# Kernel tuning notes

Measured on AMD Instinct MI355X. Metric: run time of the kernel, lower is better.

## Reference

```python
import jax, jax.numpy as jnp
from jax import lax
import numpy as np

B, T, F, H, C = 2048, 200, 64, 128, 1
IN = 2 * F + H  # GRUCell input size


def setup_inputs() -> dict:
    key = jax.random.key(0)
    ks = jax.random.split(key, 16)
    sd_h = 1.0 / np.sqrt(H)
    sd_f = 1.0 / np.sqrt(F)
    sd_g = 1.0 / np.sqrt(H)
    return {
        "values": jax.random.normal(ks[0], (B, T, F), jnp.float32),
        "masks": jnp.round(jax.random.uniform(ks[1], (B, T, F), jnp.float32)),
        "deltas": jax.random.uniform(ks[2], (B, T, F), jnp.float32),
        "x_locf": jax.random.normal(ks[3], (B, T, F), jnp.float32),
        "emp_mean": jax.random.normal(ks[4], (F,), jnp.float32),
        "Wdh": jax.random.uniform(ks[5], (H, F), jnp.float32, -sd_h, sd_h),
        "bdh": jax.random.uniform(ks[6], (H,), jnp.float32, -sd_h, sd_h),
        "Wdx": jax.random.uniform(ks[7], (F, F), jnp.float32, -sd_f, sd_f),
        "bdx": jax.random.uniform(ks[8], (F,), jnp.float32, -sd_f, sd_f),
        "w_ih": jax.random.uniform(ks[9], (3 * H, IN), jnp.float32, -sd_g, sd_g),
        "w_hh": jax.random.uniform(ks[10], (3 * H, H), jnp.float32, -sd_g, sd_g),
        "b_ih": jax.random.uniform(ks[11], (3 * H,), jnp.float32, -sd_g, sd_g),
        "b_hh": jax.random.uniform(ks[12], (3 * H,), jnp.float32, -sd_g, sd_g),
        "Wc": jax.random.uniform(ks[13], (C, H), jnp.float32, -sd_g, sd_g),
        "bc": jax.random.uniform(ks[14], (C,), jnp.float32, -sd_g, sd_g),
    }


def reference(values, masks, deltas, x_locf, emp_mean,
              Wdh, bdh, Wdx, bdx, w_ih, w_hh, b_ih, b_hh, Wc, bc):
    # GRU-D forward: sequential scan over time with temporal decay gating.
    eye = jnp.eye(Wdx.shape[0], dtype=Wdx.dtype)
    Wdx_diag = Wdx * eye  # diag=True TemporalDecay

    def step(h, inp):
        x, m, d, xl = inp  # each [B, F]
        gamma_h = jnp.exp(-jax.nn.relu(d @ Wdh.T + bdh))   # [B, H]
        gamma_x = jnp.exp(-jax.nn.relu(d @ Wdx_diag.T + bdx))  # [B, F]
        h = h * gamma_h
        x_h = gamma_x * xl + (1.0 - gamma_x) * emp_mean
        x_rep = m * x + (1.0 - m) * x_h
        inputs = jnp.concatenate([x_rep, h, m], axis=1)    # [B, 2F+H]
        gi = inputs @ w_ih.T + b_ih                        # [B, 3H]
        gh = h @ w_hh.T + b_hh                             # [B, 3H]
        i_r, i_z, i_n = jnp.split(gi, 3, axis=1)
        h_r, h_z, h_n = jnp.split(gh, 3, axis=1)
        r = jax.nn.sigmoid(i_r + h_r)
        z = jax.nn.sigmoid(i_z + h_z)
        n = jnp.tanh(i_n + r * h_n)
        h_new = (1.0 - z) * n + z * h
        return h_new, None

    xs = (values.transpose(1, 0, 2), masks.transpose(1, 0, 2),
          deltas.transpose(1, 0, 2), x_locf.transpose(1, 0, 2))
    h0 = jnp.zeros((values.shape[0], Wdh.shape[0]), values.dtype)
    h_final, _ = lax.scan(step, h0, xs)
    logits = h_final @ Wc.T + bc
    return jax.nn.sigmoid(logits)
```

## Files before the change

### kernel.cpp

```cpp
#include <hip/hip_runtime.h>
#include <hip/hip_bf16.h>

#define Bsz 2048
#define Tn  200
#define Fn  64
#define Hn  128
#define INn 256
#define Gn  384
#define BBn 8

typedef __bf16 bf16x8 __attribute__((ext_vector_type(8)));
typedef float  f32x4  __attribute__((ext_vector_type(4)));

__device__ __forceinline__ float sigm(float x)  { return 1.f / (1.f + __expf(-x)); }
__device__ __forceinline__ float tanh_(float x) { return 1.f - 2.f / (__expf(2.f * x) + 1.f); }

__global__ __launch_bounds__(512, 2) void grud_scan(
    const float* __restrict__ values, const float* __restrict__ masks,
    const float* __restrict__ deltas, const float* __restrict__ x_locf,
    const float* __restrict__ emp_mean,
    const float* __restrict__ Wdh, const float* __restrict__ bdh,
    const float* __restrict__ Wdx, const float* __restrict__ bdx,
    const float* __restrict__ w_ih, const float* __restrict__ w_hh,
    const float* __restrict__ b_ih, const float* __restrict__ b_hh,
    const float* __restrict__ Wc, const float* __restrict__ bc,
    float* __restrict__ out)
{
    __shared__ __align__(16) __bf16 in_bf[16][INn + 8];
    __shared__ __align__(16) __bf16 d_bf[16][Fn + 8];
    __shared__ float h_lds[BBn][Hn];
    __shared__ float gi_lds[BBn][Gn + 1];
    __shared__ float gh_lds[BBn][Gn + 1];
    __shared__ float bih_s[Gn], bhh_s[Gn], bdh_s[Hn];
    __shared__ float wdxd_s[Fn], bdx_s[Fn], emp_s[Fn];

    const int tid  = threadIdx.x;
    const int w    = tid >> 6;
    const int lane = tid & 63;
    const int ncol = lane & 15;
    const int kg   = lane >> 4;
    const int b0   = blockIdx.x * BBn;

    for (int i = tid; i < 16 * (INn + 8); i += 512) ((__bf16*)in_bf)[i] = (__bf16)0.f;
    for (int i = tid; i < 16 * (Fn + 8);  i += 512) ((__bf16*)d_bf)[i]  = (__bf16)0.f;
    for (int i = tid; i < BBn * Hn;       i += 512) ((float*)h_lds)[i]  = 0.f;
    for (int i = tid; i < Gn; i += 512) { bih_s[i] = b_ih[i]; bhh_s[i] = b_hh[i]; }
    for (int i = tid; i < Hn; i += 512) bdh_s[i] = bdh[i];
    for (int i = tid; i < Fn; i += 512) {
        wdxd_s[i] = Wdx[i * Fn + i];
        bdx_s[i]  = bdx[i];
        emp_s[i]  = emp_mean[i];
    }

    bf16x8 wih[3][8], whh[3][4], wdhf[2];
    #pragma unroll
    for (int nt = 0; nt < 3; ++nt) {
        const int c = w * 48 + nt * 16 + ncol;
        #pragma unroll
        for (int kc = 0; kc < 8; ++kc) {
            const float* p = w_ih + (size_t)c * INn + kc * 32 + kg * 8;
            bf16x8 v;
            #pragma unroll
            for (int e = 0; e < 8; ++e) v[e] = (__bf16)p[e];
            wih[nt][kc] = v;
        }
        #pragma unroll
        for (int kc = 0; kc < 4; ++kc) {
            const float* p = w_hh + (size_t)c * Hn + kc * 32 + kg * 8;
            bf16x8 v;
            #pragma unroll
            for (int e = 0; e < 8; ++e) v[e] = (__bf16)p[e];
            whh[nt][kc] = v;
        }
    }
    {
        const int c = w * 16 + ncol;
        #pragma unroll
        for (int kc = 0; kc < 2; ++kc) {
            const float* p = Wdh + (size_t)c * Fn + kc * 32 + kg * 8;
            bf16x8 v;
            #pragma unroll
            for (int e = 0; e < 8; ++e) v[e] = (__bf16)p[e];
            wdhf[kc] = v;
        }
    }

    __syncthreads();

    const int r_ld = w;
    const int f_ld = lane;
    size_t base0 = ((size_t)(b0 + r_ld) * Tn + 0) * Fn + f_ld;
    float x_c = values[base0], m_c = masks[base0], d_c = deltas[base0], xl_c = x_locf[base0];

    const f32x4 fz = {0.f, 0.f, 0.f, 0.f};

    for (int t = 0; t < Tn; ++t) {
        {
            float gx = __expf(-fmaxf(d_c * wdxd_s[f_ld] + bdx_s[f_ld], 0.f));
            float xh = gx * xl_c + (1.f - gx) * emp_s[f_ld];
            float xr = m_c * x_c + (1.f - m_c) * xh;
            in_bf[r_ld][f_ld]           = (__bf16)xr;
            in_bf[r_ld][Fn + Hn + f_ld] = (__bf16)m_c;
            d_bf[r_ld][f_ld]            = (__bf16)d_c;
        }
        {
            int tn = (t + 1 < Tn) ? t + 1 : Tn - 1;
            size_t base = ((size_t)(b0 + r_ld) * Tn + tn) * Fn + f_ld;
            x_c = values[base]; m_c = masks[base]; d_c = deltas[base]; xl_c = x_locf[base];
        }
        __syncthreads();

        {
            bf16x8 a0 = *(const bf16x8*)&d_bf[ncol][kg * 8];
            bf16x8 a1 = *(const bf16x8*)&d_bf[ncol][32 + kg * 8];
            f32x4 acc = fz;
            acc = __builtin_amdgcn_mfma_f32_16x16x32_bf16(a0, wdhf[0], acc, 0, 0, 0);
            acc = __builtin_amdgcn_mfma_f32_16x16x32_bf16(a1, wdhf[1], acc, 0, 0, 0);
            const int col = w * 16 + ncol;
            #pragma unroll
            for (int i = 0; i < 4; ++i) {
                int row = kg * 4 + i;
                if (row < BBn) {
                    float g  = __expf(-fmaxf(acc[i] + bdh_s[col], 0.f));
                    float hv = h_lds[row][col] * g;
                    h_lds[row][col]      = hv;
                    in_bf[row][Fn + col] = (__bf16)hv;
                }
            }
        }
        __syncthreads();

        {
            bf16x8 af[8];
            #pragma unroll
            for (int kc = 0; kc < 8; ++kc)
                af[kc] = *(const bf16x8*)&in_bf[ncol][kc * 32 + kg * 8];
            f32x4 gacc[3], hacc[3];
            #pragma unroll
            for (int nt = 0; nt < 3; ++nt) { gacc[nt] = fz; hacc[nt] = fz; }
            #pragma unroll
            for (int kc = 0; kc < 8; ++kc)
                #pragma unroll
                for (int nt = 0; nt < 3; ++nt)
                    gacc[nt] = __builtin_amdgcn_mfma_f32_16x16x32_bf16(af[kc], wih[nt][kc], gacc[nt], 0, 0, 0);
            #pragma unroll
            for (int kc = 0; kc < 4; ++kc)
                #pragma unroll
                for (int nt = 0; nt < 3; ++nt)
                    hacc[nt] = __builtin_amdgcn_mfma_f32_16x16x32_bf16(af[kc + 2], whh[nt][kc], hacc[nt], 0, 0, 0);
            #pragma unroll
            for (int nt = 0; nt < 3; ++nt)
                #pragma unroll
                for (int i = 0; i < 4; ++i) {
                    int row = kg * 4 + i;
                    if (row < BBn) {
                        int c = w * 48 + nt * 16 + ncol;
                        gi_lds[row][c] = gacc[nt][i];
                        gh_lds[row][c] = hacc[nt][i];
                    }
                }
        }
        __syncthreads();

        #pragma unroll
        for (int it = 0; it < 2; ++it) {
            int idx = tid + it * 512;
            int r = idx >> 7, j = idx & 127;
            float rg = sigm(gi_lds[r][j] + bih_s[j] + gh_lds[r][j] + bhh_s[j]);
            float zg = sigm(gi_lds[r][Hn + j] + bih_s[Hn + j] + gh_lds[r][Hn + j] + bhh_s[Hn + j]);
            float hn = gh_lds[r][2 * Hn + j] + bhh_s[2 * Hn + j];
            float ng = tanh_(gi_lds[r][2 * Hn + j] + bih_s[2 * Hn + j] + rg * hn);
            float ho = h_lds[r][j];
            h_lds[r][j] = (1.f - zg) * ng + zg * ho;
        }
        __syncthreads();
    }

    if (tid < BBn) {
        float acc = bc[0];
        #pragma unroll 8
        for (int j = 0; j < Hn; ++j) acc += h_lds[tid][j] * Wc[j];
        out[b0 + tid] = sigm(acc);
    }
}

extern "C" void kernel_launch(void* const* d_in, const int* in_sizes, int n_in,
                              void* d_out, int out_size, void* d_ws, size_t ws_size,
                              hipStream_t stream)
{
    (void)in_sizes; (void)n_in; (void)out_size; (void)d_ws; (void)ws_size;
    grud_scan<<<dim3(Bsz / BBn), dim3(512), 0, stream>>>(
        (const float*)d_in[0],  (const float*)d_in[1],  (const float*)d_in[2],
        (const float*)d_in[3],  (const float*)d_in[4],  (const float*)d_in[5],
        (const float*)d_in[6],  (const float*)d_in[7],  (const float*)d_in[8],
        (const float*)d_in[9],  (const float*)d_in[10], (const float*)d_in[11],
        (const float*)d_in[12], (const float*)d_in[13], (const float*)d_in[14],
        (float*)d_out);
}
```

Before: 677.9 us.

## Keep hidden state in registers and cut per-step barriers from four to two

Reassigns gate columns so each wave owns matching r/z/n columns for 16 hidden units, which lets the GRU gate math run directly on MFMA accumulators and keep h in registers instead of going through gi/gh/h arrays in LDS. The delta tile is double-buffered so the decay MFMA for the next step needs no extra barrier, leaving two __syncthreads per timestep instead of four. Biases and decay parameters move from shared memory into registers. This raises register pressure under the 512-thread, 2-block launch bounds, and the gate math now runs on half the lanes (kg<2).

```diff
diff --git a/kernel.cpp b/kernel.cpp
--- a/kernel.cpp
+++ b/kernel.cpp
@@ -6,7 +6,6 @@
 #define Fn  64
 #define Hn  128
 #define INn 256
-#define Gn  384
 #define BBn 8
 
 typedef __bf16 bf16x8 __attribute__((ext_vector_type(8)));
@@ -26,13 +25,9 @@
     const float* __restrict__ Wc, const float* __restrict__ bc,
     float* __restrict__ out)
 {
-    __shared__ __align__(16) __bf16 in_bf[16][INn + 8];
-    __shared__ __align__(16) __bf16 d_bf[16][Fn + 8];
-    __shared__ float h_lds[BBn][Hn];
-    __shared__ float gi_lds[BBn][Gn + 1];
-    __shared__ float gh_lds[BBn][Gn + 1];
-    __shared__ float bih_s[Gn], bhh_s[Gn], bdh_s[Hn];
-    __shared__ float wdxd_s[Fn], bdx_s[Fn], emp_s[Fn];
+    __shared__ __align__(16) __bf16 in_bf[16][264];
+    __shared__ __align__(16) __bf16 d_bf[2][16][72];
+    __shared__ float h_fin[BBn][Hn];
 
     const int tid  = threadIdx.x;
     const int w    = tid >> 6;
@@ -41,21 +36,16 @@
     const int kg   = lane >> 4;
     const int b0   = blockIdx.x * BBn;
 
-    for (int i = tid; i < 16 * (INn + 8); i += 512) ((__bf16*)in_bf)[i] = (__bf16)0.f;
-    for (int i = tid; i < 16 * (Fn + 8);  i += 512) ((__bf16*)d_bf)[i]  = (__bf16)0.f;
-    for (int i = tid; i < BBn * Hn;       i += 512) ((float*)h_lds)[i]  = 0.f;
-    for (int i = tid; i < Gn; i += 512) { bih_s[i] = b_ih[i]; bhh_s[i] = b_hh[i]; }
-    for (int i = tid; i < Hn; i += 512) bdh_s[i] = bdh[i];
-    for (int i = tid; i < Fn; i += 512) {
-        wdxd_s[i] = Wdx[i * Fn + i];
-        bdx_s[i]  = bdx[i];
-        emp_s[i]  = emp_mean[i];
-    }
+    for (int i = tid; i < 16 * 264;    i += 512) ((__bf16*)in_bf)[i] = (__bf16)0.f;
+    for (int i = tid; i < 2 * 16 * 72; i += 512) ((__bf16*)d_bf)[i]  = (__bf16)0.f;
 
     bf16x8 wih[3][8], whh[3][4], wdhf[2];
+    float bih_r[3], bhh_r[3];
     #pragma unroll
     for (int nt = 0; nt < 3; ++nt) {
-        const int c = w * 48 + nt * 16 + ncol;
+        const int c = nt * Hn + w * 16 + ncol;
+        bih_r[nt] = b_ih[c];
+        bhh_r[nt] = b_hh[c];
         #pragma unroll
         for (int kc = 0; kc < 8; ++kc) {
             const float* p = w_ih + (size_t)c * INn + kc * 32 + kg * 8;
@@ -73,113 +63,103 @@
             whh[nt][kc] = v;
         }
     }
-    {
-        const int c = w * 16 + ncol;
+    const int ch = w * 16 + ncol;
+    const float bdh_r = bdh[ch];
+    #pragma unroll
+    for (int kc = 0; kc < 2; ++kc) {
+        const float* p = Wdh + (size_t)ch * Fn + kc * 32 + kg * 8;
+        bf16x8 v;
         #pragma unroll
-        for (int kc = 0; kc < 2; ++kc) {
-            const float* p = Wdh + (size_t)c * Fn + kc * 32 + kg * 8;
-            bf16x8 v;
-            #pragma unroll
-            for (int e = 0; e < 8; ++e) v[e] = (__bf16)p[e];
-            wdhf[kc] = v;
-        }
+        for (int e = 0; e < 8; ++e) v[e] = (__bf16)p[e];
+        wdhf[kc] = v;
     }
 
+    const int r_ld = w, f_ld = lane;
+    const float wdxd_r = Wdx[(size_t)f_ld * Fn + f_ld];
+    const float bdx_r  = bdx[f_ld];
+    const float emp_r  = emp_mean[f_ld];
+    const float* vp = values + (size_t)(b0 + r_ld) * Tn * Fn + f_ld;
+    const float* mp = masks  + (size_t)(b0 + r_ld) * Tn * Fn + f_ld;
+    const float* dp = deltas + (size_t)(b0 + r_ld) * Tn * Fn + f_ld;
+    const float* lp = x_locf + (size_t)(b0 + r_ld) * Tn * Fn + f_ld;
+
+    float h_reg[4] = {0.f, 0.f, 0.f, 0.f};
+
+    float x_c = vp[0], m_c = mp[0], d_c = dp[0], xl_c = lp[0];
+    d_bf[0][r_ld][f_ld] = (__bf16)d_c;
     __syncthreads();
-
-    const int r_ld = w;
-    const int f_ld = lane;
-    size_t base0 = ((size_t)(b0 + r_ld) * Tn + 0) * Fn + f_ld;
-    float x_c = values[base0], m_c = masks[base0], d_c = deltas[base0], xl_c = x_locf[base0];
 
     const f32x4 fz = {0.f, 0.f, 0.f, 0.f};
 
     for (int t = 0; t < Tn; ++t) {
-        {
-            float gx = __expf(-fmaxf(d_c * wdxd_s[f_ld] + bdx_s[f_ld], 0.f));
-            float xh = gx * xl_c + (1.f - gx) * emp_s[f_ld];
-            float xr = m_c * x_c + (1.f - m_c) * xh;
-            in_bf[r_ld][f_ld]           = (__bf16)xr;
-            in_bf[r_ld][Fn + Hn + f_ld] = (__bf16)m_c;
-            d_bf[r_ld][f_ld]            = (__bf16)d_c;
+        const int cur = t & 1;
+
+        bf16x8 a0 = *(const bf16x8*)&d_bf[cur][ncol][kg * 8];
+        bf16x8 a1 = *(const bf16x8*)&d_bf[cur][ncol][32 + kg * 8];
+        f32x4 acc = fz;
+        acc = __builtin_amdgcn_mfma_f32_16x16x32_bf16(a0, wdhf[0], acc, 0, 0, 0);
+        acc = __builtin_amdgcn_mfma_f32_16x16x32_bf16(a1, wdhf[1], acc, 0, 0, 0);
+        if (kg < 2) {
+            #pragma unroll
+            for (int i = 0; i < 4; ++i) {
+                float g  = __expf(-fmaxf(acc[i] + bdh_r, 0.f));
+                float hv = h_reg[i] * g;
+                h_reg[i] = hv;
+                in_bf[kg * 4 + i][Fn + ch] = (__bf16)hv;
+            }
         }
         {
-            int tn = (t + 1 < Tn) ? t + 1 : Tn - 1;
-            size_t base = ((size_t)(b0 + r_ld) * Tn + tn) * Fn + f_ld;
-            x_c = values[base]; m_c = masks[base]; d_c = deltas[base]; xl_c = x_locf[base];
+            float gx = __expf(-fmaxf(d_c * wdxd_r + bdx_r, 0.f));
+            float xh = gx * xl_c + (1.f - gx) * emp_r;
+            float xr = m_c * x_c + (1.f - m_c) * xh;
+            in_bf[r_ld][f_ld]            = (__bf16)xr;
+            in_bf[r_ld][Fn + Hn + f_ld]  = (__bf16)m_c;
         }
+        const int off = (t + 1 < Tn) ? (t + 1) * Fn : t * Fn;
+        float x_n = vp[off], m_n = mp[off], d_n = dp[off], xl_n = lp[off];
         __syncthreads();
 
-        {
-            bf16x8 a0 = *(const bf16x8*)&d_bf[ncol][kg * 8];
-            bf16x8 a1 = *(const bf16x8*)&d_bf[ncol][32 + kg * 8];
-            f32x4 acc = fz;
-            acc = __builtin_amdgcn_mfma_f32_16x16x32_bf16(a0, wdhf[0], acc, 0, 0, 0);
-            acc = __builtin_amdgcn_mfma_f32_16x16x32_bf16(a1, wdhf[1], acc, 0, 0, 0);
-            const int col = w * 16 + ncol;
+        bf16x8 af[8];
+        #pragma unroll
+        for (int kc = 0; kc < 8; ++kc)
+            af[kc] = *(const bf16x8*)&in_bf[ncol][kc * 32 + kg * 8];
+        f32x4 gacc[3], hacc[3];
+        #pragma unroll
+        for (int nt = 0; nt < 3; ++nt) { gacc[nt] = fz; hacc[nt] = fz; }
+        #pragma unroll
+        for (int kc = 0; kc < 8; ++kc)
+            #pragma unroll
+            for (int nt = 0; nt < 3; ++nt)
+                gacc[nt] = __builtin_amdgcn_mfma_f32_16x16x32_bf16(af[kc], wih[nt][kc], gacc[nt], 0, 0, 0);
+        #pragma unroll
+        for (int kc = 0; kc < 4; ++kc)
+            #pragma unroll
+            for (int nt = 0; nt < 3; ++nt)
+                hacc[nt] = __builtin_amdgcn_mfma_f32_16x16x32_bf16(af[kc + 2], whh[nt][kc], hacc[nt], 0, 0, 0);
+        if (kg < 2) {
             #pragma unroll
             for (int i = 0; i < 4; ++i) {
-                int row = kg * 4 + i;
-                if (row < BBn) {
-                    float g  = __expf(-fmaxf(acc[i] + bdh_s[col], 0.f));
-                    float hv = h_lds[row][col] * g;
-                    h_lds[row][col]      = hv;
-                    in_bf[row][Fn + col] = (__bf16)hv;
-                }
+                float rg = sigm(gacc[0][i] + bih_r[0] + hacc[0][i] + bhh_r[0]);
+                float zg = sigm(gacc[1][i] + bih_r[1] + hacc[1][i] + bhh_r[1]);
+                float hn = hacc[2][i] + bhh_r[2];
+                float ng = tanh_(gacc[2][i] + bih_r[2] + rg * hn);
+                h_reg[i] = (1.f - zg) * ng + zg * h_reg[i];
             }
         }
-        __syncthreads();
-
-        {
-            bf16x8 af[8];
-            #pragma unroll
-            for (int kc = 0; kc < 8; ++kc)
-                af[kc] = *(const bf16x8*)&in_bf[ncol][kc * 32 + kg * 8];
-            f32x4 gacc[3], hacc[3];
-            #pragma unroll
-            for (int nt = 0; nt < 3; ++nt) { gacc[nt] = fz; hacc[nt] = fz; }
-            #pragma unroll
-            for (int kc = 0; kc < 8; ++kc)
-                #pragma unroll
-                for (int nt = 0; nt < 3; ++nt)
-                    gacc[nt] = __builtin_amdgcn_mfma_f32_16x16x32_bf16(af[kc], wih[nt][kc], gacc[nt], 0, 0, 0);
-            #pragma unroll
-            for (int kc = 0; kc < 4; ++kc)
-                #pragma unroll
-                for (int nt = 0; nt < 3; ++nt)
-                    hacc[nt] = __builtin_amdgcn_mfma_f32_16x16x32_bf16(af[kc + 2], whh[nt][kc], hacc[nt], 0, 0, 0);
-            #pragma unroll
-            for (int nt = 0; nt < 3; ++nt)
-                #pragma unroll
-                for (int i = 0; i < 4; ++i) {
-                    int row = kg * 4 + i;
-                    if (row < BBn) {
-                        int c = w * 48 + nt * 16 + ncol;
-                        gi_lds[row][c] = gacc[nt][i];
-                        gh_lds[row][c] = hacc[nt][i];
-                    }
-                }
-        }
-        __syncthreads();
-
-        #pragma unroll
-        for (int it = 0; it < 2; ++it) {
-            int idx = tid + it * 512;
-            int r = idx >> 7, j = idx & 127;
-            float rg = sigm(gi_lds[r][j] + bih_s[j] + gh_lds[r][j] + bhh_s[j]);
-            float zg = sigm(gi_lds[r][Hn + j] + bih_s[Hn + j] + gh_lds[r][Hn + j] + bhh_s[Hn + j]);
-            float hn = gh_lds[r][2 * Hn + j] + bhh_s[2 * Hn + j];
-            float ng = tanh_(gi_lds[r][2 * Hn + j] + bih_s[2 * Hn + j] + rg * hn);
-            float ho = h_lds[r][j];
-            h_lds[r][j] = (1.f - zg) * ng + zg * ho;
-        }
+        x_c = x_n; m_c = m_n; d_c = d_n; xl_c = xl_n;
+        d_bf[cur ^ 1][r_ld][f_ld] = (__bf16)d_n;
         __syncthreads();
     }
 
+    if (kg < 2) {
+        #pragma unroll
+        for (int i = 0; i < 4; ++i) h_fin[kg * 4 + i][ch] = h_reg[i];
+    }
+    __syncthreads();
     if (tid < BBn) {
         float acc = bc[0];
         #pragma unroll 8
-        for (int j = 0; j < Hn; ++j) acc += h_lds[tid][j] * Wc[j];
+        for (int j = 0; j < Hn; ++j) acc += h_fin[tid][j] * Wc[j];
         out[b0 + tid] = sigm(acc);
     }
 }
```

Result: faster. 621.5 us (-8.3%).
